# Kernel optimization log

Hardware: AMD Instinct MI355X
Metric: run time of the kernel (lower is better)

The kernel has to match this reference:

```python
import jax, jax.numpy as jnp
import numpy as np

DIM, SEQ, HEADS = 1024, 2048, 8
HEAD_DIM = DIM // HEADS


def setup_inputs() -> dict:
    key = jax.random.key(0)
    ks = jax.random.split(key, 8)
    x = jax.random.normal(ks[0], (4, SEQ, DIM), dtype=jnp.float32)
    # Linear weights stored [in, out]; y = x @ W + b (same math as torch Linear).
    Wk = jax.random.normal(ks[1], (DIM, DIM), dtype=jnp.float32) * (DIM ** -0.5)
    bk = jnp.zeros((DIM,), dtype=jnp.float32)
    Wv = jax.random.normal(ks[2], (DIM, DIM), dtype=jnp.float32) * (DIM ** -0.5)
    bv = jnp.zeros((DIM,), dtype=jnp.float32)
    # learned AFT position bias [heads, seq, seq]; small scale keeps exp stable
    w_aft = jax.random.normal(ks[3], (HEADS, SEQ, SEQ), dtype=jnp.float32) * 0.1
    Wo = jax.random.normal(ks[4], (DIM, DIM), dtype=jnp.float32) * (DIM ** -0.5)
    bo = jnp.zeros((DIM,), dtype=jnp.float32)
    return {"x": x, "Wk": Wk, "bk": bk, "Wv": Wv, "bv": bv,
            "w_aft": w_aft, "Wo": Wo, "bo": bo}


def reference(x, Wk, bk, Wv, bv, w_aft, Wo, bo):
    N, S, _ = x.shape
    k = (x @ Wk + bk).reshape(N, S, HEADS, HEAD_DIM)
    v = (x @ Wv + bv).reshape(N, S, HEADS, HEAD_DIM)
    ek = jnp.exp(k)  # [N,S,H,D]
    # causal mask: position t attends to i <= t; exp(w+k) = exp(w)*exp(k)
    causal = jnp.tril(jnp.ones((S, S), dtype=bool))
    ew = jnp.where(causal[None, :, :], jnp.exp(w_aft), 0.0)  # [H,T,S]
    num = jnp.einsum('hts,nshd->nthd', ew, ek * v)  # [N,T,H,D]
    den = jnp.einsum('hts,nshd->nthd', ew, ek)      # [N,T,H,D]
    aft = (num / den).reshape(N, S, DIM)
    return aft @ Wo + bo
```

## Files before the change

### kernel.cpp

```cpp
#include <hip/hip_runtime.h>
#include <hip/hip_bf16.h>
#include <stdint.h>

#define DIM 1024
#define SEQ 2048
#define NB 4
#define HEADS 8
#define HD 128
#define ROWS (NB*SEQ)

typedef __attribute__((ext_vector_type(8))) short bf16x8;
typedef __attribute__((ext_vector_type(4))) float f32x4;

#define VMCNT(n) asm volatile("s_waitcnt vmcnt(" #n ")" ::: "memory")
#define SBAR()   __builtin_amdgcn_s_barrier()
#define SCHED0() __builtin_amdgcn_sched_barrier(0)

static __device__ __forceinline__ unsigned short f2bf(float f){
  union { float f; unsigned int u; } x; x.f = f;
  unsigned int r = x.u + 0x7fffu + ((x.u >> 16) & 1u);
  return (unsigned short)(r >> 16);
}

static __device__ __forceinline__ void gld_lds16(const void* g, void* l){
  __builtin_amdgcn_global_load_lds(
      (const __attribute__((address_space(1))) void*)g,
      (__attribute__((address_space(3))) void*)l,
      16, 0, 0);
}

__global__ void k_prep(const float* __restrict__ x,
                       const float* __restrict__ Wk, const float* __restrict__ Wv,
                       const float* __restrict__ Wo, const float* __restrict__ waft,
                       unsigned short* __restrict__ xb,
                       unsigned short* __restrict__ Tk, unsigned short* __restrict__ Tv,
                       unsigned short* __restrict__ To, unsigned short* __restrict__ ewb){
  __shared__ float tile[64][65];
  const int B = blockIdx.x;
  const int tid = threadIdx.x;
  if (B < 2048){
    for (int i = B*256 + tid; i < ROWS*DIM/4; i += 2048*256){
      const float4 v = reinterpret_cast<const float4*>(x)[i];
      ushort4 o;
      o.x = f2bf(v.x); o.y = f2bf(v.y); o.z = f2bf(v.z); o.w = f2bf(v.w);
      reinterpret_cast<ushort4*>(xb)[i] = o;
    }
  } else if (B < 2816){
    const int D = B - 2048;
    const int z = D >> 8;
    const int rem = D & 255;
    const int bo = (rem & 15) * 64;
    const int bi = (rem >> 4) * 64;
    const float* W = (z == 0) ? Wk : (z == 1) ? Wv : Wo;
    unsigned short* WT = (z == 0) ? Tk : (z == 1) ? Tv : To;
    #pragma unroll
    for (int it = 0; it < 16; ++it){
      int f = it*256 + tid;
      int r = f >> 6, c = f & 63;
      tile[r][c] = W[(size_t)(bi + r) * DIM + bo + c];
    }
    __syncthreads();
    #pragma unroll
    for (int it = 0; it < 16; ++it){
      int f = it*256 + tid;
      int r = f >> 6, c = f & 63;
      WT[(size_t)(bo + r) * DIM + bi + c] = f2bf(tile[c][r]);
    }
  } else {
    const int row = (B - 2816) * 4 + (tid >> 6);
    const int lane = tid & 63;
    const int t = row & 2047;
    const int h = row >> 11;
    const float* src = waft + ((size_t)h*SEQ + t) * SEQ;
    unsigned short* dst = ewb + ((size_t)h*SEQ + t) * SEQ;
    const int smax4 = ((t & ~127) + 128) >> 2;
    for (int i = lane; i < smax4; i += 64){
      const float4 w4 = reinterpret_cast<const float4*>(src)[i];
      const int s = i * 4;
      ushort4 o;
      o.x = (s+0 <= t) ? f2bf(__expf(w4.x)) : (unsigned short)0;
      o.y = (s+1 <= t) ? f2bf(__expf(w4.y)) : (unsigned short)0;
      o.z = (s+2 <= t) ? f2bf(__expf(w4.z)) : (unsigned short)0;
      o.w = (s+3 <= t) ? f2bf(__expf(w4.w)) : (unsigned short)0;
      reinterpret_cast<ushort4*>(dst)[i] = o;
    }
  }
}

__global__ __launch_bounds__(512) void k_proj(
    const unsigned short* __restrict__ xb,
    const unsigned short* __restrict__ wkt,
    const unsigned short* __restrict__ wvt,
    const float* __restrict__ bk,
    const float* __restrict__ bv,
    unsigned short* __restrict__ ekb)
{
  __shared__ __align__(16) char smem[131072];
  unsigned short* Asl = (unsigned short*)smem;
  unsigned short* Bsl = (unsigned short*)(smem + 65536);
  float* xch = (float*)smem;

  const int tid  = threadIdx.x;
  const int lane = tid & 63;
  const int lo   = lane & 15;
  const int hi   = lane >> 4;
  const int wid  = tid >> 6;
  const int wm   = wid >> 2;
  const int wn   = wid & 3;
  const int D    = blockIdx.x;
  const int mb   = D >> 3;
  const int cb   = D & 7;
  const int row0 = mb * 256;
  const int col0k = cb * 128;

  f32x4 acc[8][4] = {};

  auto stage_unit = [&](int kt, int slot, int u){
    const int half = u & 1;
    const bool isB = (u >> 1) != 0;
    unsigned short* lb = (isB ? Bsl : Asl) + slot*(256*64) + half*(128*64);
    const unsigned short* gb;
    if (!isB)           gb = xb  + (size_t)(row0 + half*128)*DIM + kt*64;
    else if (half == 0) gb = wkt + (size_t)col0k*DIM + kt*64;
    else                gb = wvt + (size_t)col0k*DIM + kt*64;
    #pragma unroll
    for (int it = 0; it < 2; ++it){
      const int po = (it*512 + tid)*16;
      const int r  = po >> 7;
      const int k2 = (po & 127) ^ ((r & 7) << 4);
      gld_lds16(gb + (size_t)r*DIM + (k2 >> 1), (char*)lb + po);
    }
  };

  #pragma unroll
  for (int u = 0; u < 4; ++u) stage_unit(0, 0, u);

  for (int t = 0; t < 16; ++t){
    const int s = t & 1;
    const char* Ab = (const char*)(Asl + s*(256*64));
    const char* Bb = (const char*)(Bsl + s*(256*64));
    bf16x8 b[4][2];
    #pragma unroll
    for (int ph = 0; ph < 2; ++ph){
      if (t + 1 < 16){
        stage_unit(t + 1, s ^ 1, ph*2);
        stage_unit(t + 1, s ^ 1, ph*2 + 1);
      }
      if (ph == 0){
        if (t + 1 < 16) { VMCNT(4); } else { VMCNT(0); }
      }
      SCHED0();
      SBAR();
      SCHED0();
      if (ph == 0){
        #pragma unroll
        for (int nf = 0; nf < 4; ++nf){
          const int R = wn*64 + nf*16 + lo;
          #pragma unroll
          for (int ks = 0; ks < 2; ++ks){
            const int K2 = (ks*64 + hi*16) ^ ((R & 7) << 4);
            b[nf][ks] = *reinterpret_cast<const bf16x8*>(Bb + R*128 + K2);
          }
        }
      }
      bf16x8 a[4][2];
      #pragma unroll
      for (int mf = 0; mf < 4; ++mf){
        const int R = wm*128 + (ph*4 + mf)*16 + lo;
        #pragma unroll
        for (int ks = 0; ks < 2; ++ks){
          const int K2 = (ks*64 + hi*16) ^ ((R & 7) << 4);
          a[mf][ks] = *reinterpret_cast<const bf16x8*>(Ab + R*128 + K2);
        }
      }
      __builtin_amdgcn_s_setprio(1);
      #pragma unroll
      for (int ks = 0; ks < 2; ++ks)
        #pragma unroll
        for (int mf = 0; mf < 4; ++mf)
          #pragma unroll
          for (int nf = 0; nf < 4; ++nf)
            acc[ph*4+mf][nf] = __builtin_amdgcn_mfma_f32_16x16x32_bf16(
                a[mf][ks], b[nf][ks], acc[ph*4+mf][nf], 0, 0, 0);
      __builtin_amdgcn_s_setprio(0);
      SCHED0();
      SBAR();
    }
  }

  __syncthreads();
  if (wn >= 2){
    #pragma unroll
    for (int mf = 0; mf < 8; ++mf){
      const int rloc = wm*128 + mf*16 + hi*4;
      #pragma unroll
      for (int nf = 0; nf < 4; ++nf){
        const int cv = (wn - 2)*64 + nf*16 + lo;
        #pragma unroll
        for (int jj = 0; jj < 4; ++jj)
          xch[(size_t)(rloc + jj)*128 + cv] = acc[mf][nf][jj];
      }
    }
  }
  __syncthreads();
  if (wn < 2){
    #pragma unroll
    for (int nf = 0; nf < 4; ++nf){
      const int ck = wn*64 + nf*16 + lo;
      const int c  = col0k + ck;
      const int h  = c >> 7;
      const int d  = c & 127;
      const float bkc = bk[c];
      const float bvc = bv[c];
      #pragma unroll
      for (int mf = 0; mf < 8; ++mf){
        const int rloc = wm*128 + mf*16 + hi*4;
        const int r = row0 + rloc;
        const int n = r >> 11;
        const int sidx = r & 2047;
        ushort4 pk, pv;
        #pragma unroll
        for (int jj = 0; jj < 4; ++jj){
          const float kval = acc[mf][nf][jj] + bkc;
          const float vval = xch[(size_t)(rloc + jj)*128 + ck] + bvc;
          const float ek = __expf(kval);
          ((unsigned short*)&pk)[jj] = f2bf(ek);
          ((unsigned short*)&pv)[jj] = f2bf(ek * vval);
        }
        const size_t idx = ((size_t)h*1024 + n*256 + d) * SEQ + sidx;
        *reinterpret_cast<ushort4*>(&ekb[idx]) = pk;
        *reinterpret_cast<ushort4*>(&ekb[idx + (size_t)128*SEQ]) = pv;
      }
    }
  }
}

__global__ __launch_bounds__(512) void k_core(
    const unsigned short* __restrict__ ewb,
    const unsigned short* __restrict__ ekb,
    unsigned short* __restrict__ aftb)
{
  __shared__ __align__(16) char smem[98304];
  unsigned short* Asl = (unsigned short*)smem;
  unsigned short* Bsl = (unsigned short*)(smem + 32768);
  float* xch = (float*)smem;

  const int tid  = threadIdx.x;
  const int lane = tid & 63;
  const int lo   = lane & 15;
  const int hi   = lane >> 4;
  const int wid  = tid >> 6;
  const int wm   = wid >> 2;
  const int wn   = wid & 3;
  const int D  = blockIdx.x;
  const int h  = D & 7;
  const int r_ = D >> 3;
  const int p  = r_ >> 2;
  const int n  = r_ & 3;

  const unsigned short* slab = ekb + ((size_t)h*1024 + n*256) * SEQ;

  #pragma unroll
  for (int half = 0; half < 2; ++half){
    const int tt = half ? p : (15 - p);
    const int t0 = tt * 128;
    const int nst = 2*tt + 2;
    const unsigned short* abase = ewb + ((size_t)h*SEQ + t0) * SEQ;

    f32x4 acc[4][4] = {};

    auto stage_unit = [&](int st, int slot, int u){
      const int s0 = st * 64;
      const int po = tid * 16;
      const int r  = po >> 7;
      const int k2 = (po & 127) ^ ((r & 7) << 4);
      if (u < 2){
        unsigned short* lb = Asl + slot*(128*64) + u*(64*64);
        gld_lds16(abase + (size_t)(u*64 + r)*SEQ + s0 + (k2 >> 1), (char*)lb + po);
      } else {
        unsigned short* lb = Bsl + slot*(256*64) + (u-2)*(64*64);
        gld_lds16(slab + (size_t)((u-2)*64 + r)*SEQ + s0 + (k2 >> 1), (char*)lb + po);
      }
    };

    #pragma unroll
    for (int u = 0; u < 6; ++u) stage_unit(0, 0, u);

    for (int t = 0; t < nst; ++t){
      const int s = t & 1;
      const char* Ab = (const char*)(Asl + s*(128*64));
      const char* Bb = (const char*)(Bsl + s*(256*64));
      bf16x8 b[4][2];
      #pragma unroll
      for (int ph = 0; ph < 2; ++ph){
        if (t + 1 < nst){
          stage_unit(t + 1, s ^ 1, ph*3);
          stage_unit(t + 1, s ^ 1, ph*3 + 1);
          stage_unit(t + 1, s ^ 1, ph*3 + 2);
        }
        if (ph == 0){
          if (t + 1 < nst) { VMCNT(3); } else { VMCNT(0); }
        }
        SCHED0();
        SBAR();
        SCHED0();
        if (ph == 0){
          #pragma unroll
          for (int nf = 0; nf < 4; ++nf){
            const int R = wn*64 + nf*16 + lo;
            #pragma unroll
            for (int ks = 0; ks < 2; ++ks){
              const int K2 = (ks*64 + hi*16) ^ ((R & 7) << 4);
              b[nf][ks] = *reinterpret_cast<const bf16x8*>(Bb + R*128 + K2);
            }
          }
        }
        bf16x8 a[2][2];
        #pragma unroll
        for (int mf = 0; mf < 2; ++mf){
          const int R = wm*64 + (ph*2 + mf)*16 + lo;
          #pragma unroll
          for (int ks = 0; ks < 2; ++ks){
            const int K2 = (ks*64 + hi*16) ^ ((R & 7) << 4);
            a[mf][ks] = *reinterpret_cast<const bf16x8*>(Ab + R*128 + K2);
          }
        }
        __builtin_amdgcn_s_setprio(1);
        #pragma unroll
        for (int ks = 0; ks < 2; ++ks)
          #pragma unroll
          for (int mf = 0; mf < 2; ++mf)
            #pragma unroll
            for (int nf = 0; nf < 4; ++nf)
              acc[ph*2+mf][nf] = __builtin_amdgcn_mfma_f32_16x16x32_bf16(
                  a[mf][ks], b[nf][ks], acc[ph*2+mf][nf], 0, 0, 0);
        __builtin_amdgcn_s_setprio(0);
        SCHED0();
        SBAR();
      }
    }

    __syncthreads();
    if (wn >= 2){
      #pragma unroll
      for (int mf = 0; mf < 4; ++mf){
        const int rloc = wm*64 + mf*16 + hi*4;
        #pragma unroll
        for (int nf = 0; nf < 4; ++nf){
          const int dv = (wn - 2)*64 + nf*16 + lo;
          #pragma unroll
          for (int jj = 0; jj < 4; ++jj)
            xch[(size_t)(rloc + jj)*129 + dv] = acc[mf][nf][jj];
        }
      }
    }
    __syncthreads();
    if (wn < 2){
      #pragma unroll
      for (int nf = 0; nf < 4; ++nf){
        const int d = wn*64 + nf*16 + lo;
        #pragma unroll
        for (int mf = 0; mf < 4; ++mf){
          const int rloc = wm*64 + mf*16 + hi*4;
          #pragma unroll
          for (int jj = 0; jj < 4; ++jj){
            const int t = t0 + rloc + jj;
            const float num = xch[(size_t)(rloc + jj)*129 + d];
            aftb[((size_t)n*SEQ + t)*DIM + h*HD + d] = f2bf(num / acc[mf][nf][jj]);
          }
        }
      }
    }
    __syncthreads();
  }
}

__global__ __launch_bounds__(512) void k_out(
    const unsigned short* __restrict__ aftb,
    const unsigned short* __restrict__ wot,
    const float* __restrict__ bo,
    float* __restrict__ out)
{
  __shared__ __align__(16) char smem[98304];
  unsigned short* Asl = (unsigned short*)smem;
  unsigned short* Bsl = (unsigned short*)(smem + 32768);

  const int tid  = threadIdx.x;
  const int lane = tid & 63;
  const int lo   = lane & 15;
  const int hi   = lane >> 4;
  const int wid  = tid >> 6;
  const int wm   = wid >> 2;
  const int wn   = wid & 3;
  const int D    = blockIdx.x;
  const int row0 = (D >> 2) * 128;
  const int col0 = (D & 3) * 256;

  f32x4 acc[4][4] = {};

  auto stage_unit = [&](int kt, int slot, int u){
    const int po = tid * 16;
    const int r  = po >> 7;
    const int k2 = (po & 127) ^ ((r & 7) << 4);
    if (u < 2){
      unsigned short* lb = Asl + slot*(128*64) + u*(64*64);
      gld_lds16(aftb + (size_t)(row0 + u*64 + r)*DIM + kt*64 + (k2 >> 1), (char*)lb + po);
    } else {
      unsigned short* lb = Bsl + slot*(256*64) + (u-2)*(64*64);
      gld_lds16(wot + (size_t)(col0 + (u-2)*64 + r)*DIM + kt*64 + (k2 >> 1), (char*)lb + po);
    }
  };

  #pragma unroll
  for (int u = 0; u < 6; ++u) stage_unit(0, 0, u);

  for (int t = 0; t < 16; ++t){
    const int s = t & 1;
    const char* Ab = (const char*)(Asl + s*(128*64));
    const char* Bb = (const char*)(Bsl + s*(256*64));
    bf16x8 b[4][2];
    #pragma unroll
    for (int ph = 0; ph < 2; ++ph){
      if (t + 1 < 16){
        stage_unit(t + 1, s ^ 1, ph*3);
        stage_unit(t + 1, s ^ 1, ph*3 + 1);
        stage_unit(t + 1, s ^ 1, ph*3 + 2);
      }
      if (ph == 0){
        if (t + 1 < 16) { VMCNT(3); } else { VMCNT(0); }
      }
      SCHED0();
      SBAR();
      SCHED0();
      if (ph == 0){
        #pragma unroll
        for (int nf = 0; nf < 4; ++nf){
          const int R = wn*64 + nf*16 + lo;
          #pragma unroll
          for (int ks = 0; ks < 2; ++ks){
            const int K2 = (ks*64 + hi*16) ^ ((R & 7) << 4);
            b[nf][ks] = *reinterpret_cast<const bf16x8*>(Bb + R*128 + K2);
          }
        }
      }
      bf16x8 a[2][2];
      #pragma unroll
      for (int mf = 0; mf < 2; ++mf){
        const int R = wm*64 + (ph*2 + mf)*16 + lo;
        #pragma unroll
        for (int ks = 0; ks < 2; ++ks){
          const int K2 = (ks*64 + hi*16) ^ ((R & 7) << 4);
          a[mf][ks] = *reinterpret_cast<const bf16x8*>(Ab + R*128 + K2);
        }
      }
      __builtin_amdgcn_s_setprio(1);
      #pragma unroll
      for (int ks = 0; ks < 2; ++ks)
        #pragma unroll
        for (int mf = 0; mf < 2; ++mf)
          #pragma unroll
          for (int nf = 0; nf < 4; ++nf)
            acc[ph*2+mf][nf] = __builtin_amdgcn_mfma_f32_16x16x32_bf16(
                a[mf][ks], b[nf][ks], acc[ph*2+mf][nf], 0, 0, 0);
      __builtin_amdgcn_s_setprio(0);
      SCHED0();
      SBAR();
    }
  }

  #pragma unroll
  for (int nf = 0; nf < 4; ++nf){
    const int c = col0 + wn*64 + nf*16 + lo;
    const float boc = bo[c];
    #pragma unroll
    for (int mf = 0; mf < 4; ++mf){
      #pragma unroll
      for (int jj = 0; jj < 4; ++jj){
        const int r = row0 + wm*64 + mf*16 + hi*4 + jj;
        out[(size_t)r*DIM + c] = acc[mf][nf][jj] + boc;
      }
    }
  }
}

extern "C" void kernel_launch(void* const* d_in, const int* in_sizes, int n_in,
                              void* d_out, int out_size, void* d_ws, size_t ws_size,
                              hipStream_t stream){
  const float* x    = (const float*)d_in[0];
  const float* Wk   = (const float*)d_in[1];
  const float* bk   = (const float*)d_in[2];
  const float* Wv   = (const float*)d_in[3];
  const float* bv   = (const float*)d_in[4];
  const float* waft = (const float*)d_in[5];
  const float* Wo   = (const float*)d_in[6];
  const float* bo   = (const float*)d_in[7];
  float* out = (float*)d_out;

  char* w = (char*)d_ws;
  unsigned short* xb   = (unsigned short*)w; w += (size_t)ROWS*DIM*2;
  unsigned short* wkt  = (unsigned short*)w; w += (size_t)DIM*DIM*2;
  unsigned short* wvt  = (unsigned short*)w; w += (size_t)DIM*DIM*2;
  unsigned short* wot  = (unsigned short*)w; w += (size_t)DIM*DIM*2;
  unsigned short* ekb  = (unsigned short*)w; w += (size_t)HEADS*1024*SEQ*2;
  unsigned short* aftb = (unsigned short*)w; w += (size_t)ROWS*DIM*2;
  unsigned short* ewb  = (unsigned short*)w; w += (size_t)HEADS*SEQ*SEQ*2;

  k_prep<<<6912, 256, 0, stream>>>(x, Wk, Wv, Wo, waft, xb, wkt, wvt, wot, ewb);
  k_proj<<<256, 512, 0, stream>>>(xb, wkt, wvt, bk, bv, ekb);
  k_core<<<256, 512, 0, stream>>>(ewb, ekb, aftb);
  k_out<<<256, 512, 0, stream>>>(aftb, wot, bo, out);
}
```

Before: 142.5 us.

## Collapse two-phase GEMM k-loop into one barrier pair per iteration

Restructures the main loop in all three GEMM kernels so each k-tile iteration uses one wait/barrier at the top and one at the end, instead of a barrier pair per half-phase. The second half of the next tile's global-to-LDS prefetch is now issued after the first A-fragment reads, and the two MFMA halves run back to back without an intermediate barrier. The aim is to cut workgroup barrier stalls and let the compiler overlap the second half's LDS reads with MFMA work. It holds both A-fragment sets' lifetimes closer together, which may raise register pressure, and the issue pattern of the later prefetch changes.

```diff
diff --git a/kernel.cpp b/kernel.cpp
--- a/kernel.cpp
+++ b/kernel.cpp
@@ -137,55 +137,75 @@
 
   for (int t = 0; t < 16; ++t){
     const int s = t & 1;
+    const bool nxt = (t + 1 < 16);
     const char* Ab = (const char*)(Asl + s*(256*64));
     const char* Bb = (const char*)(Bsl + s*(256*64));
+    if (nxt){
+      stage_unit(t + 1, s ^ 1, 0);
+      stage_unit(t + 1, s ^ 1, 1);
+      VMCNT(4);
+    } else {
+      VMCNT(0);
+    }
+    SCHED0();
+    SBAR();
+    SCHED0();
     bf16x8 b[4][2];
     #pragma unroll
-    for (int ph = 0; ph < 2; ++ph){
-      if (t + 1 < 16){
-        stage_unit(t + 1, s ^ 1, ph*2);
-        stage_unit(t + 1, s ^ 1, ph*2 + 1);
-      }
-      if (ph == 0){
-        if (t + 1 < 16) { VMCNT(4); } else { VMCNT(0); }
-      }
-      SCHED0();
-      SBAR();
-      SCHED0();
-      if (ph == 0){
-        #pragma unroll
-        for (int nf = 0; nf < 4; ++nf){
-          const int R = wn*64 + nf*16 + lo;
-          #pragma unroll
-          for (int ks = 0; ks < 2; ++ks){
-            const int K2 = (ks*64 + hi*16) ^ ((R & 7) << 4);
-            b[nf][ks] = *reinterpret_cast<const bf16x8*>(Bb + R*128 + K2);
-          }
-        }
-      }
-      bf16x8 a[4][2];
-      #pragma unroll
-      for (int mf = 0; mf < 4; ++mf){
-        const int R = wm*128 + (ph*4 + mf)*16 + lo;
-        #pragma unroll
-        for (int ks = 0; ks < 2; ++ks){
-          const int K2 = (ks*64 + hi*16) ^ ((R & 7) << 4);
-          a[mf][ks] = *reinterpret_cast<const bf16x8*>(Ab + R*128 + K2);
-        }
-      }
-      __builtin_amdgcn_s_setprio(1);
-      #pragma unroll
-      for (int ks = 0; ks < 2; ++ks)
-        #pragma unroll
-        for (int mf = 0; mf < 4; ++mf)
-          #pragma unroll
-          for (int nf = 0; nf < 4; ++nf)
-            acc[ph*4+mf][nf] = __builtin_amdgcn_mfma_f32_16x16x32_bf16(
-                a[mf][ks], b[nf][ks], acc[ph*4+mf][nf], 0, 0, 0);
-      __builtin_amdgcn_s_setprio(0);
-      SCHED0();
-      SBAR();
-    }
+    for (int nf = 0; nf < 4; ++nf){
+      const int R = wn*64 + nf*16 + lo;
+      #pragma unroll
+      for (int ks = 0; ks < 2; ++ks){
+        const int K2 = (ks*64 + hi*16) ^ ((R & 7) << 4);
+        b[nf][ks] = *reinterpret_cast<const bf16x8*>(Bb + R*128 + K2);
+      }
+    }
+    bf16x8 a0[4][2];
+    #pragma unroll
+    for (int mf = 0; mf < 4; ++mf){
+      const int R = wm*128 + mf*16 + lo;
+      #pragma unroll
+      for (int ks = 0; ks < 2; ++ks){
+        const int K2 = (ks*64 + hi*16) ^ ((R & 7) << 4);
+        a0[mf][ks] = *reinterpret_cast<const bf16x8*>(Ab + R*128 + K2);
+      }
+    }
+    if (nxt){
+      stage_unit(t + 1, s ^ 1, 2);
+      stage_unit(t + 1, s ^ 1, 3);
+    }
+    __builtin_amdgcn_s_setprio(1);
+    #pragma unroll
+    for (int ks = 0; ks < 2; ++ks)
+      #pragma unroll
+      for (int mf = 0; mf < 4; ++mf)
+        #pragma unroll
+        for (int nf = 0; nf < 4; ++nf)
+          acc[mf][nf] = __builtin_amdgcn_mfma_f32_16x16x32_bf16(
+              a0[mf][ks], b[nf][ks], acc[mf][nf], 0, 0, 0);
+    __builtin_amdgcn_s_setprio(0);
+    bf16x8 a1[4][2];
+    #pragma unroll
+    for (int mf = 0; mf < 4; ++mf){
+      const int R = wm*128 + (4 + mf)*16 + lo;
+      #pragma unroll
+      for (int ks = 0; ks < 2; ++ks){
+        const int K2 = (ks*64 + hi*16) ^ ((R & 7) << 4);
+        a1[mf][ks] = *reinterpret_cast<const bf16x8*>(Ab + R*128 + K2);
+      }
+    }
+    __builtin_amdgcn_s_setprio(1);
+    #pragma unroll
+    for (int ks = 0; ks < 2; ++ks)
+      #pragma unroll
+      for (int mf = 0; mf < 4; ++mf)
+        #pragma unroll
+        for (int nf = 0; nf < 4; ++nf)
+          acc[4+mf][nf] = __builtin_amdgcn_mfma_f32_16x16x32_bf16(
+              a1[mf][ks], b[nf][ks], acc[4+mf][nf], 0, 0, 0);
+    __builtin_amdgcn_s_setprio(0);
+    SCHED0();
+    SBAR();
   }
 
   __syncthreads();
@@ -288,56 +308,77 @@
 
     for (int t = 0; t < nst; ++t){
       const int s = t & 1;
+      const bool nxt = (t + 1 < nst);
       const char* Ab = (const char*)(Asl + s*(128*64));
       const char* Bb = (const char*)(Bsl + s*(256*64));
+      if (nxt){
+        stage_unit(t + 1, s ^ 1, 0);
+        stage_unit(t + 1, s ^ 1, 1);
+        stage_unit(t + 1, s ^ 1, 2);
+        VMCNT(3);
+      } else {
+        VMCNT(0);
+      }
+      SCHED0();
+      SBAR();
+      SCHED0();
       bf16x8 b[4][2];
       #pragma unroll
-      for (int ph = 0; ph < 2; ++ph){
-        if (t + 1 < nst){
-          stage_unit(t + 1, s ^ 1, ph*3);
-          stage_unit(t + 1, s ^ 1, ph*3 + 1);
-          stage_unit(t + 1, s ^ 1, ph*3 + 2);
+      for (int nf = 0; nf < 4; ++nf){
+        const int R = wn*64 + nf*16 + lo;
+        #pragma unroll
+        for (int ks = 0; ks < 2; ++ks){
+          const int K2 = (ks*64 + hi*16) ^ ((R & 7) << 4);
+          b[nf][ks] = *reinterpret_cast<const bf16x8*>(Bb + R*128 + K2);
         }
-        if (ph == 0){
-          if (t + 1 < nst) { VMCNT(3); } else { VMCNT(0); }
+      }
+      bf16x8 a0[2][2];
+      #pragma unroll
+      for (int mf = 0; mf < 2; ++mf){
+        const int R = wm*64 + mf*16 + lo;
+        #pragma unroll
+        for (int ks = 0; ks < 2; ++ks){
+          const int K2 = (ks*64 + hi*16) ^ ((R & 7) << 4);
+          a0[mf][ks] = *reinterpret_cast<const bf16x8*>(Ab + R*128 + K2);
         }
-        SCHED0();
-        SBAR();
-        SCHED0();
-        if (ph == 0){
+      }
+      if (nxt){
+        stage_unit(t + 1, s ^ 1, 3);
+        stage_unit(t + 1, s ^ 1, 4);
+        stage_unit(t + 1, s ^ 1, 5);
+      }
+      __builtin_amdgcn_s_setprio(1);
+      #pragma unroll
+      for (int ks = 0; ks < 2; ++ks)
+        #pragma unroll
+        for (int mf = 0; mf < 2; ++mf)
           #pragma unroll
-          for (int nf = 0; nf < 4; ++nf){
-            const int R = wn*64 + nf*16 + lo;
-            #pragma unroll
-            for (int ks = 0; ks < 2; ++ks){
-              const int K2 = (ks*64 + hi*16) ^ ((R & 7) << 4);
-              b[nf][ks] = *reinterpret_cast<const bf16x8*>(Bb + R*128 + K2);
-            }
-          }
+          for (int nf = 0; nf < 4; ++nf)
+            acc[mf][nf] = __builtin_amdgcn_mfma_f32_16x16x32_bf16(
+                a0[mf][ks], b[nf][ks], acc[mf][nf], 0, 0, 0);
+      __builtin_amdgcn_s_setprio(0);
+      bf16x8 a1[2][2];
+      #pragma unroll
+      for (int mf = 0; mf < 2; ++mf){
+        const int R = wm*64 + (2 + mf)*16 + lo;
+        #pragma unroll
+        for (int ks = 0; ks < 2; ++ks){
+          const int K2 = (ks*64 + hi*16) ^ ((R & 7) << 4);
+          a1[mf][ks] = *reinterpret_cast<const bf16x8*>(Ab + R*128 + K2);
         }
-        bf16x8 a[2][2];
-        #pragma unroll
-        for (int mf = 0; mf < 2; ++mf){
-          const int R = wm*64 + (ph*2 + mf)*16 + lo;
+      }
+      __builtin_amdgcn_s_setprio(1);
+      #pragma unroll
+      for (int ks = 0; ks < 2; ++ks)
+        #pragma unroll
+        for (int mf = 0; mf < 2; ++mf)
           #pragma unroll
-          for (int ks = 0; ks < 2; ++ks){
-            const int K2 = (ks*64 + hi*16) ^ ((R & 7) << 4);
-            a[mf][ks] = *reinterpret_cast<const bf16x8*>(Ab + R*128 + K2);
-          }
-        }
-        __builtin_amdgcn_s_setprio(1);
-        #pragma unroll
-        for (int ks = 0; ks < 2; ++ks)
-          #pragma unroll
-          for (int mf = 0; mf < 2; ++mf)
-            #pragma unroll
-            for (int nf = 0; nf < 4; ++nf)
-              acc[ph*2+mf][nf] = __builtin_amdgcn_mfma_f32_16x16x32_bf16(
-                  a[mf][ks], b[nf][ks], acc[ph*2+mf][nf], 0, 0, 0);
-        __builtin_amdgcn_s_setprio(0);
-        SCHED0();
-        SBAR();
-      }
+          for (int nf = 0; nf < 4; ++nf)
+            acc[2+mf][nf] = __builtin_amdgcn_mfma_f32_16x16x32_bf16(
+                a1[mf][ks], b[nf][ks], acc[2+mf][nf], 0, 0, 0);
+      __builtin_amdgcn_s_setprio(0);
+      SCHED0();
+      SBAR();
     }
 
     __syncthreads();
@@ -416,56 +457,77 @@
 
   for (int t = 0; t < 16; ++t){
     const int s = t & 1;
+    const bool nxt = (t + 1 < 16);
     const char* Ab = (const char*)(Asl + s*(128*64));
     const char* Bb = (const char*)(Bsl + s*(256*64));
+    if (nxt){
+      stage_unit(t + 1, s ^ 1, 0);
+      stage_unit(t + 1, s ^ 1, 1);
+      stage_unit(t + 1, s ^ 1, 2);
+      VMCNT(3);
+    } else {
+      VMCNT(0);
+    }
+    SCHED0();
+    SBAR();
+    SCHED0();
     bf16x8 b[4][2];
     #pragma unroll
-    for (int ph = 0; ph < 2; ++ph){
-      if (t + 1 < 16){
-        stage_unit(t + 1, s ^ 1, ph*3);
-        stage_unit(t + 1, s ^ 1, ph*3 + 1);
-        stage_unit(t + 1, s ^ 1, ph*3 + 2);
-      }
-      if (ph == 0){
-        if (t + 1 < 16) { VMCNT(3); } else { VMCNT(0); }
-      }
-      SCHED0();
-      SBAR();
-      SCHED0();
-      if (ph == 0){
-        #pragma unroll
-        for (int nf = 0; nf < 4; ++nf){
-          const int R = wn*64 + nf*16 + lo;
-          #pragma unroll
-          for (int ks = 0; ks < 2; ++ks){
-            const int K2 = (ks*64 + hi*16) ^ ((R & 7) << 4);
-            b[nf][ks] = *reinterpret_cast<const bf16x8*>(Bb + R*128 + K2);
-          }
-        }
-      }
-      bf16x8 a[2][2];
-      #pragma unroll
-      for (int mf = 0; mf < 2; ++mf){
-        const int R = wm*64 + (ph*2 + mf)*16 + lo;
-        #pragma unroll
-        for (int ks = 0; ks < 2; ++ks){
-          const int K2 = (ks*64 + hi*16) ^ ((R & 7) << 4);
-          a[mf][ks] = *reinterpret_cast<const bf16x8*>(Ab + R*128 + K2);
-        }
-      }
-      __builtin_amdgcn_s_setprio(1);
-      #pragma unroll
-      for (int ks = 0; ks < 2; ++ks)
-        #pragma unroll
-        for (int mf = 0; mf < 2; ++mf)
-          #pragma unroll
-          for (int nf = 0; nf < 4; ++nf)
-            acc[ph*2+mf][nf] = __builtin_amdgcn_mfma_f32_16x16x32_bf16(
-                a[mf][ks], b[nf][ks], acc[ph*2+mf][nf], 0, 0, 0);
-      __builtin_amdgcn_s_setprio(0);
-      SCHED0();
-      SBAR();
-    }
+    for (int nf = 0; nf < 4; ++nf){
+      const int R = wn*64 + nf*16 + lo;
+      #pragma unroll
+      for (int ks = 0; ks < 2; ++ks){
+        const int K2 = (ks*64 + hi*16) ^ ((R & 7) << 4);
+        b[nf][ks] = *reinterpret_cast<const bf16x8*>(Bb + R*128 + K2);
+      }
+    }
+    bf16x8 a0[2][2];
+    #pragma unroll
+    for (int mf = 0; mf < 2; ++mf){
+      const int R = wm*64 + mf*16 + lo;
+      #pragma unroll
+      for (int ks = 0; ks < 2; ++ks){
+        const int K2 = (ks*64 + hi*16) ^ ((R & 7) << 4);
+        a0[mf][ks] = *reinterpret_cast<const bf16x8*>(Ab + R*128 + K2);
+      }
+    }
+    if (nxt){
+      stage_unit(t + 1, s ^ 1, 3);
+      stage_unit(t + 1, s ^ 1, 4);
+      stage_unit(t + 1, s ^ 1, 5);
+    }
+    __builtin_amdgcn_s_setprio(1);
+    #pragma unroll
+    for (int ks = 0; ks < 2; ++ks)
+      #pragma unroll
+      for (int mf = 0; mf < 2; ++mf)
+        #pragma unroll
+        for (int nf = 0; nf < 4; ++nf)
+          acc[mf][nf] = __builtin_amdgcn_mfma_f32_16x16x32_bf16(
+              a0[mf][ks], b[nf][ks], acc[mf][nf], 0, 0, 0);
+    __builtin_amdgcn_s_setprio(0);
+    bf16x8 a1[2][2];
+    #pragma unroll
+    for (int mf = 0; mf < 2; ++mf){
+      const int R = wm*64 + (2 + mf)*16 + lo;
+      #pragma unroll
+      for (int ks = 0; ks < 2; ++ks){
+        const int K2 = (ks*64 + hi*16) ^ ((R & 7) << 4);
+        a1[mf][ks] = *reinterpret_cast<const bf16x8*>(Ab + R*128 + K2);
+      }
+    }
+    __builtin_amdgcn_s_setprio(1);
+    #pragma unroll
+    for (int ks = 0; ks < 2; ++ks)
+      #pragma unroll
+      for (int mf = 0; mf < 2; ++mf)
+        #pragma unroll
+        for (int nf = 0; nf < 4; ++nf)
+          acc[2+mf][nf] = __builtin_amdgcn_mfma_f32_16x16x32_bf16(
+              a1[mf][ks], b[nf][ks], acc[2+mf][nf], 0, 0, 0);
+    __builtin_amdgcn_s_setprio(0);
+    SCHED0();
+    SBAR();
   }
 
   #pragma unroll
```

Result: faster. 139.5 us (-2.1%).
